# Kernel optimization log

Measured on AMD Instinct MI355X. Metric: run time of the kernel, lower is better.

## Reference

```python
import jax, jax.numpy as jnp
import numpy as np


def _fps_indices(xyz, num_points):
    """Furthest point sampling. xyz: [B, N, 3] -> indices [B, num_points] (int32)."""
    B, N, _ = xyz.shape

    def step(carry, _):
        dist, farthest = carry                                   # dist: [B, N], farthest: [B]
        centroid = jnp.take_along_axis(xyz, farthest[:, None, None], axis=1)  # [B, 1, 3]
        d = jnp.sum((xyz - centroid) ** 2, axis=-1)              # [B, N]
        dist = jnp.minimum(dist, d)
        nxt = jnp.argmax(dist, axis=-1).astype(jnp.int32)        # [B]
        return (dist, nxt), farthest

    init = (jnp.full((B, N), jnp.inf, dtype=xyz.dtype),
            jnp.zeros((B,), dtype=jnp.int32))                    # convention: start at index 0
    _, idxs = jax.lax.scan(step, init, None, length=num_points)  # [num_points, B]
    return idxs.T                                                # [B, num_points]


def setup_inputs() -> dict:
    key = jax.random.key(0)
    B, C, N = 16, 3, 131072
    points = jax.random.normal(key, (B, C, N), dtype=jnp.float32)
    return {"points": points, "num_points": 2048}


def reference(points, num_points):
    # points: [B, 3, N] channels-first, as in the torch module
    xyz = jnp.transpose(points, (0, 2, 1))                       # [B, N, 3]
    idx = _fps_indices(xyz, num_points)                          # [B, num_points]
    # fps_gather_by_index: gather along the point dim of the channels-first tensor
    new_points = jnp.take_along_axis(points, idx[:, None, :], axis=2)  # [B, 3, num_points]
    return new_points
```

## Files before the change

kernel.cpp:

```cpp
#include <hip/hip_runtime.h>
#include <stdint.h>


#define NBATCH    16
#define NPTS      131072
#define SUBBLOCKS 16
#define NTHREADS  1024
#define CHUNK     8192
#define HALF      4096

typedef unsigned long long u64;

__device__ __forceinline__ u64 umax64(u64 a, u64 b) { return a > b ? a : b; }

__global__ __launch_bounds__(NTHREADS, 4)
void fps_kernel(const float* __restrict__ points,
                float* __restrict__ out,
                u64* __restrict__ slots, int M)
{
  __shared__ u64 wkeys[NTHREADS / 64];
  __shared__ float winC[3];

  const int bid   = blockIdx.x;
  const int xcd   = bid & 7;
  const int ord   = bid >> 3;
  const int batch = xcd * 2 + (ord >> 4);
  const int sub   = ord & 15;
  const int tid   = threadIdx.x;
  const int wave  = tid >> 6;
  const int lane  = tid & 63;

  const float* __restrict__ px = points + (size_t)batch * 3 * NPTS;
  const float* __restrict__ py = px + NPTS;
  const float* __restrict__ pz = px + 2 * NPTS;
  float* outb = out + (size_t)batch * 3 * M;
  u64* bslots = slots + (size_t)batch * 2 * SUBBLOCKS;

  const int cbase = sub * CHUNK;
  const int g0 = cbase + (tid << 2);
  const int g1 = g0 + HALF;

  float4 A0 = *(const float4*)(px + g0);
  float4 B0 = *(const float4*)(py + g0);
  float4 C0 = *(const float4*)(pz + g0);
  float4 A1 = *(const float4*)(px + g1);
  float4 B1 = *(const float4*)(py + g1);
  float4 C1 = *(const float4*)(pz + g1);
  float x0=A0.x, x1=A0.y, x2=A0.z, x3=A0.w, x4=A1.x, x5=A1.y, x6=A1.z, x7=A1.w;
  float y0=B0.x, y1=B0.y, y2=B0.z, y3=B0.w, y4=B1.x, y5=B1.y, y6=B1.z, y7=B1.w;
  float z0=C0.x, z1=C0.y, z2=C0.z, z3=C0.w, z4=C1.x, z5=C1.y, z6=C1.z, z7=C1.w;
  asm volatile("" :
    "+v"(x0),"+v"(x1),"+v"(x2),"+v"(x3),"+v"(x4),"+v"(x5),"+v"(x6),"+v"(x7),
    "+v"(y0),"+v"(y1),"+v"(y2),"+v"(y3),"+v"(y4),"+v"(y5),"+v"(y6),"+v"(y7),
    "+v"(z0),"+v"(z1),"+v"(z2),"+v"(z3),"+v"(z4),"+v"(z5),"+v"(z6),"+v"(z7));

  float d0, d1, d2, d3, d4, d5, d6, d7;
  d0 = d1 = d2 = d3 = d4 = d5 = d6 = d7 = __builtin_inff();

  if (sub == 0 && tid == 0) {
    outb[0]     = px[0];
    outb[M]     = py[0];
    outb[2 * M] = pz[0];
  }
  float cx = px[0], cy = py[0], cz = pz[0];

  for (int t = 1; t < M; ++t) {
    float best = -1.0f;
    int bidx = 0;
#define STEP(XX, YY, ZZ, DREG, IDX) { \
    float dx = __fsub_rn((XX), cx); \
    float dy = __fsub_rn((YY), cy); \
    float dz = __fsub_rn((ZZ), cz); \
    float dd = __builtin_fmaf(dz, dz, __builtin_fmaf(dy, dy, __fmul_rn(dx, dx))); \
    DREG = DREG < dd ? DREG : dd; \
    if (DREG > best) { best = DREG; bidx = (IDX); } }
    STEP(x0, y0, z0, d0, g0 + 0)
    STEP(x1, y1, z1, d1, g0 + 1)
    STEP(x2, y2, z2, d2, g0 + 2)
    STEP(x3, y3, z3, d3, g0 + 3)
    STEP(x4, y4, z4, d4, g1 + 0)
    STEP(x5, y5, z5, d5, g1 + 1)
    STEP(x6, y6, z6, d6, g1 + 2)
    STEP(x7, y7, z7, d7, g1 + 3)

    u64 key = ((u64)__float_as_uint(best) << 17) | (u64)((NPTS - 1) - bidx);

#pragma unroll
    for (int m = 32; m >= 1; m >>= 1) {
      u64 o = __shfl_xor(key, m, 64);
      key = umax64(key, o);
    }
    if (lane == 0) wkeys[wave] = key;
    __syncthreads();

    if (wave == 0) {
      u64 k = wkeys[lane & 15];
#pragma unroll
      for (int m = 8; m >= 1; m >>= 1) {
        u64 o = __shfl_xor(k, m, 64);
        k = umax64(k, o);
      }
      u64* par = bslots + (size_t)(t & 1) * SUBBLOCKS;
      if (lane == 0) {
        __hip_atomic_store(par + sub, ((u64)t << 49) | k,
                           __ATOMIC_RELAXED, __HIP_MEMORY_SCOPE_AGENT);
      }
      const u64* pp = par + (lane & 15);

      asm volatile("s_waitcnt vmcnt(0)" ::: "memory");

      u64 va, vb, v;
      asm volatile("global_load_dwordx2 %0, %1, off sc0 sc1"
                   : "=v"(va) : "v"(pp) : "memory");
      asm volatile("global_load_dwordx2 %0, %1, off sc0 sc1"
                   : "=v"(vb) : "v"(pp) : "memory");
      for (;;) {
        asm volatile("s_waitcnt vmcnt(1)" ::: "memory");
        __builtin_amdgcn_sched_barrier(0);
        if (__ballot((unsigned)(va >> 49) == (unsigned)t) == ~0ull) { v = va; break; }
        asm volatile("global_load_dwordx2 %0, %1, off sc0 sc1"
                     : "=v"(va) : "v"(pp) : "memory");
        asm volatile("s_waitcnt vmcnt(1)" ::: "memory");
        __builtin_amdgcn_sched_barrier(0);
        if (__ballot((unsigned)(vb >> 49) == (unsigned)t) == ~0ull) { v = vb; break; }
        asm volatile("global_load_dwordx2 %0, %1, off sc0 sc1"
                     : "=v"(vb) : "v"(pp) : "memory");
      }

      int cidx = (NPTS - 1) - (int)(v & 0x1FFFF);
      float qx = 0.f, qy = 0.f, qz = 0.f;
      if (lane < 16) { qx = px[cidx]; qy = py[cidx]; qz = pz[cidx]; }
      u64 kk = v;
#pragma unroll
      for (int m = 8; m >= 1; m >>= 1) {
        u64 o = __shfl_xor(kk, m, 64);
        kk = umax64(kk, o);
      }
      if (lane < 16 && v == kk) { winC[0] = qx; winC[1] = qy; winC[2] = qz; }
      asm volatile("s_waitcnt vmcnt(0)" :: "v"(va), "v"(vb) : "memory");
    }
    __syncthreads();

    cx = winC[0]; cy = winC[1]; cz = winC[2];
    if (sub == 0 && tid == 0) {
      outb[t]         = cx;
      outb[M + t]     = cy;
      outb[2 * M + t] = cz;
    }
  }
}

extern "C" void kernel_launch(void* const* d_in, const int* in_sizes, int n_in,
                              void* d_out, int out_size, void* d_ws, size_t ws_size,
                              hipStream_t stream) {
  (void)in_sizes; (void)n_in; (void)ws_size;
  const float* points = (const float*)d_in[0];
  float* out = (float*)d_out;
  u64* slots = (u64*)d_ws;
  const int M = out_size / (NBATCH * 3);

  hipMemsetAsync(d_ws, 0, (size_t)NBATCH * 2 * SUBBLOCKS * sizeof(u64), stream);

  hipLaunchKernelGGL(fps_kernel, dim3(NBATCH * SUBBLOCKS), dim3(NTHREADS), 0,
                     stream, points, out, slots, M);
}
```

Baseline: 4.206 ms.

## Shrink blocks to 256 threads holding 32 points each in registers

Each block now runs 256 threads instead of 1024, and each thread keeps 32 points in registers (8 float4 groups at stride 1024) instead of 8. The block-level reduction shrinks from 16 waves to 4, which cuts the cost of the per-iteration __syncthreads and the cross-wave max. In exchange each thread does four times the serial distance and argmax work per step and needs many more VGPRs, while the grid size stays the same.

```diff
diff --git a/kernel.cpp b/kernel.cpp
--- a/kernel.cpp
+++ b/kernel.cpp
@@ -5,20 +5,21 @@
 #define NBATCH    16
 #define NPTS      131072
 #define SUBBLOCKS 16
-#define NTHREADS  1024
+#define NTHREADS  256
+#define NWAVES    (NTHREADS / 64)
 #define CHUNK     8192
-#define HALF      4096
+#define GSTRIDE   1024
 
 typedef unsigned long long u64;
 
 __device__ __forceinline__ u64 umax64(u64 a, u64 b) { return a > b ? a : b; }
 
-__global__ __launch_bounds__(NTHREADS, 4)
+__global__ __launch_bounds__(NTHREADS, 1)
 void fps_kernel(const float* __restrict__ points,
                 float* __restrict__ out,
                 u64* __restrict__ slots, int M)
 {
-  __shared__ u64 wkeys[NTHREADS / 64];
+  __shared__ u64 wkeys[NWAVES];
   __shared__ float winC[3];
 
   const int bid   = blockIdx.x;
@@ -37,25 +38,24 @@
   u64* bslots = slots + (size_t)batch * 2 * SUBBLOCKS;
 
   const int cbase = sub * CHUNK;
-  const int g0 = cbase + (tid << 2);
-  const int g1 = g0 + HALF;
+  const int gbase = cbase + (tid << 2);
 
-  float4 A0 = *(const float4*)(px + g0);
-  float4 B0 = *(const float4*)(py + g0);
-  float4 C0 = *(const float4*)(pz + g0);
-  float4 A1 = *(const float4*)(px + g1);
-  float4 B1 = *(const float4*)(py + g1);
-  float4 C1 = *(const float4*)(pz + g1);
-  float x0=A0.x, x1=A0.y, x2=A0.z, x3=A0.w, x4=A1.x, x5=A1.y, x6=A1.z, x7=A1.w;
-  float y0=B0.x, y1=B0.y, y2=B0.z, y3=B0.w, y4=B1.x, y5=B1.y, y6=B1.z, y7=B1.w;
-  float z0=C0.x, z1=C0.y, z2=C0.z, z3=C0.w, z4=C1.x, z5=C1.y, z6=C1.z, z7=C1.w;
-  asm volatile("" :
-    "+v"(x0),"+v"(x1),"+v"(x2),"+v"(x3),"+v"(x4),"+v"(x5),"+v"(x6),"+v"(x7),
-    "+v"(y0),"+v"(y1),"+v"(y2),"+v"(y3),"+v"(y4),"+v"(y5),"+v"(y6),"+v"(y7),
-    "+v"(z0),"+v"(z1),"+v"(z2),"+v"(z3),"+v"(z4),"+v"(z5),"+v"(z6),"+v"(z7));
+  float4 X[8], Y[8], Z[8], D[8];
+#pragma unroll
+  for (int g = 0; g < 8; ++g) {
+    X[g] = *(const float4*)(px + gbase + (g << 10));
+    Y[g] = *(const float4*)(py + gbase + (g << 10));
+    Z[g] = *(const float4*)(pz + gbase + (g << 10));
+  }
+#define PIN(G) asm volatile("" : \
+    "+v"(X[G].x),"+v"(X[G].y),"+v"(X[G].z),"+v"(X[G].w), \
+    "+v"(Y[G].x),"+v"(Y[G].y),"+v"(Y[G].z),"+v"(Y[G].w), \
+    "+v"(Z[G].x),"+v"(Z[G].y),"+v"(Z[G].z),"+v"(Z[G].w));
+  PIN(0) PIN(1) PIN(2) PIN(3) PIN(4) PIN(5) PIN(6) PIN(7)
 
-  float d0, d1, d2, d3, d4, d5, d6, d7;
-  d0 = d1 = d2 = d3 = d4 = d5 = d6 = d7 = __builtin_inff();
+#pragma unroll
+  for (int g = 0; g < 8; ++g)
+    D[g].x = D[g].y = D[g].z = D[g].w = __builtin_inff();
 
   if (sub == 0 && tid == 0) {
     outb[0]     = px[0];
@@ -66,23 +66,20 @@
 
   for (int t = 1; t < M; ++t) {
     float best = -1.0f;
-    int bidx = 0;
-#define STEP(XX, YY, ZZ, DREG, IDX) { \
-    float dx = __fsub_rn((XX), cx); \
-    float dy = __fsub_rn((YY), cy); \
-    float dz = __fsub_rn((ZZ), cz); \
+    int bj = 0;
+#define STEP1(G, C, J) { \
+    float dx = __fsub_rn(X[G].C, cx); \
+    float dy = __fsub_rn(Y[G].C, cy); \
+    float dz = __fsub_rn(Z[G].C, cz); \
     float dd = __builtin_fmaf(dz, dz, __builtin_fmaf(dy, dy, __fmul_rn(dx, dx))); \
-    DREG = DREG < dd ? DREG : dd; \
-    if (DREG > best) { best = DREG; bidx = (IDX); } }
-    STEP(x0, y0, z0, d0, g0 + 0)
-    STEP(x1, y1, z1, d1, g0 + 1)
-    STEP(x2, y2, z2, d2, g0 + 2)
-    STEP(x3, y3, z3, d3, g0 + 3)
-    STEP(x4, y4, z4, d4, g1 + 0)
-    STEP(x5, y5, z5, d5, g1 + 1)
-    STEP(x6, y6, z6, d6, g1 + 2)
-    STEP(x7, y7, z7, d7, g1 + 3)
+    float dn = D[G].C < dd ? D[G].C : dd; \
+    D[G].C = dn; \
+    if (dn > best) { best = dn; bj = 4 * (G) + (J); } }
+#define STEPG(G) STEP1(G, x, 0) STEP1(G, y, 1) STEP1(G, z, 2) STEP1(G, w, 3)
+    STEPG(0) STEPG(1) STEPG(2) STEPG(3)
+    STEPG(4) STEPG(5) STEPG(6) STEPG(7)
 
+    const int bidx = gbase + ((bj >> 2) << 10) + (bj & 3);
     u64 key = ((u64)__float_as_uint(best) << 17) | (u64)((NPTS - 1) - bidx);
 
 #pragma unroll
@@ -94,12 +91,9 @@
     __syncthreads();
 
     if (wave == 0) {
-      u64 k = wkeys[lane & 15];
-#pragma unroll
-      for (int m = 8; m >= 1; m >>= 1) {
-        u64 o = __shfl_xor(k, m, 64);
-        k = umax64(k, o);
-      }
+      u64 k = wkeys[lane & 3];
+      k = umax64(k, __shfl_xor(k, 2, 64));
+      k = umax64(k, __shfl_xor(k, 1, 64));
       u64* par = bslots + (size_t)(t & 1) * SUBBLOCKS;
       if (lane == 0) {
         __hip_atomic_store(par + sub, ((u64)t << 49) | k,
```

New measurement: 4.190 ms. No clear change (-0.4%).
